# Kernel optimization log

Hardware: AMD Instinct MI355X
Metric: run time of the kernel (lower is better)

## Reference

```python
import jax, jax.numpy as jnp
import numpy as np
import math

B, S, H = 8, 1024, 1024
NH, DH = 16, 64  # MULTI_HEAD, HIDDEN_SIZE_HEAD


def setup_inputs() -> dict:
    key = jax.random.key(0)
    ks = jax.random.split(key, 12)
    scale = 0.02
    inp = {
        "v": jax.random.normal(ks[0], (B, S, H), jnp.float32),
        "k": jax.random.normal(ks[1], (B, S, H), jnp.float32),
        "q": jax.random.normal(ks[2], (B, S, H), jnp.float32),
        # True = masked position (masked_fill semantics)
        "mask": jax.random.bernoulli(ks[3], 0.1, (B, 1, 1, S)),
        "Wq": jax.random.normal(ks[4], (H, H), jnp.float32) * scale,
        "bq": jnp.zeros((H,), jnp.float32),
        "Wk": jax.random.normal(ks[5], (H, H), jnp.float32) * scale,
        "bk": jnp.zeros((H,), jnp.float32),
        "Wv": jax.random.normal(ks[6], (H, H), jnp.float32) * scale,
        "bv": jnp.zeros((H,), jnp.float32),
        "Wm": jax.random.normal(ks[7], (H, H), jnp.float32) * scale,
        "bm": jnp.zeros((H,), jnp.float32),
    }
    return inp


def _split_heads(x):
    # [B, S, H] -> [B, NH, S, DH]
    b, s, _ = x.shape
    return x.reshape(b, s, NH, DH).transpose(0, 2, 1, 3)


def reference(v, k, q, mask, Wq, bq, Wk, bk, Wv, bv, Wm, bm):
    # QKV projections (torch Linear: x @ W.T + b)
    qh = _split_heads(q @ Wq.T + bq)  # [B, NH, S, DH]
    kh = _split_heads(k @ Wk.T + bk)
    vh = _split_heads(v @ Wv.T + bv)

    scores = jnp.einsum("bhqd,bhkd->bhqk", qh, kh) / math.sqrt(DH)
    scores = jnp.where(mask, jnp.float32(-1e9), scores)
    att = jax.nn.softmax(scores, axis=-1)
    # dropout rate 0.0 (eval mode) -> identity
    ctx = jnp.einsum("bhqk,bhkd->bhqd", att, vh)  # [B, NH, S, DH]

    b = q.shape[0]
    merged = ctx.transpose(0, 2, 1, 3).reshape(b, -1, NH * DH)  # [B, S, H]
    return merged @ Wm.T + bm
```

## Files before the change

### kernel.cpp

```cpp
#include <hip/hip_runtime.h>
#include <hip/hip_bf16.h>

#define Bn 8
#define Sn 1024
#define Hn 1024
#define NHn 16
#define DHn 64
#define Mn (Bn * Sn)

typedef unsigned short u16;
typedef short bf16x8 __attribute__((ext_vector_type(8)));
typedef unsigned short u16x4 __attribute__((ext_vector_type(4)));
typedef float f32x4 __attribute__((ext_vector_type(4)));

__device__ __forceinline__ u16 f2bf(float x) {
  union { __hip_bfloat16 h; u16 u; } cv;
  cv.h = __float2bfloat16(x);
  return cv.u;
}

__device__ __forceinline__ void async_ld16(void* lds, const void* g) {
  __builtin_amdgcn_global_load_lds(
      (const __attribute__((address_space(1))) void*)g,
      (__attribute__((address_space(3))) void*)lds, 16, 0, 0);
}

template <int CTRL>
__device__ __forceinline__ float dpp_mov(float v) {
  union { float f; int i; } a, b;
  a.f = v;
  b.i = __builtin_amdgcn_mov_dpp(a.i, CTRL, 0xF, 0xF, 1);
  return b.f;
}
__device__ __forceinline__ float row16_max(float v) {
  v = fmaxf(v, dpp_mov<0xB1>(v));
  v = fmaxf(v, dpp_mov<0x4E>(v));
  v = fmaxf(v, dpp_mov<0x124>(v));
  v = fmaxf(v, dpp_mov<0x128>(v));
  return v;
}
__device__ __forceinline__ float row16_sum(float v) {
  v += dpp_mov<0xB1>(v);
  v += dpp_mov<0x4E>(v);
  v += dpp_mov<0x124>(v);
  v += dpp_mov<0x128>(v);
  return v;
}

__global__ __launch_bounds__(256) void sniff_k(const void* __restrict__ mask,
                                               int* __restrict__ flags) {
  __shared__ int viol;
  if (threadIdx.x == 0) viol = 0;
  __syncthreads();
  const unsigned* mw = (const unsigned*)mask;
  int vb = 0;
#pragma unroll
  for (int j = 0; j < 8; ++j) {
    unsigned v = mw[threadIdx.x * 8 + j];
    if (v > 1u) vb |= 1;
    if ((v & 0xFEFEFEFEu) != 0u) vb |= 2;
    if (!(v == 0u || v == 0x3F800000u)) vb |= 4;
    unsigned h0 = v & 0xFFFFu, h1 = v >> 16;
    if (!((h0 == 0u || h0 == 0x3F80u) && (h1 == 0u || h1 == 0x3F80u))) vb |= 8;
  }
  if (vb) atomicOr(&viol, vb);
  __syncthreads();
  if (threadIdx.x == 0) {
    int mt;
    if (!(viol & 1))      mt = 0;
    else if (!(viol & 2)) mt = 1;
    else if (!(viol & 4)) mt = 3;
    else if (!(viol & 8)) mt = 2;
    else                  mt = 0;
    flags[1] = mt;
  }
}

__global__ __launch_bounds__(256) void convert3(
    const float* __restrict__ a, const float* __restrict__ b,
    const float* __restrict__ c, u16* __restrict__ da,
    u16* __restrict__ db, u16* __restrict__ dc) {
  const int seg = blockIdx.x >> 12;
  const int bid = blockIdx.x & 4095;
  const float* s = seg == 0 ? a : seg == 1 ? b : c;
  u16* d        = seg == 0 ? da : seg == 1 ? db : dc;
  const int i = (bid * 256 + threadIdx.x) * 8;
  f32x4 lo = *(const f32x4*)(s + i);
  f32x4 hi = *(const f32x4*)(s + i + 4);
  bf16x8 o;
#pragma unroll
  for (int j = 0; j < 4; ++j) { o[j] = (short)f2bf(lo[j]); o[4 + j] = (short)f2bf(hi[j]); }
  *(bf16x8*)(d + i) = o;
}

__global__ __launch_bounds__(256) void convertW(
    const float* __restrict__ a, const float* __restrict__ b,
    const float* __restrict__ c, const float* __restrict__ e,
    u16* __restrict__ da, u16* __restrict__ db,
    u16* __restrict__ dc, u16* __restrict__ de) {
  const int seg = blockIdx.x >> 9;
  const int bid = blockIdx.x & 511;
  const float* s = seg == 0 ? a : seg == 1 ? b : seg == 2 ? c : e;
  u16* d        = seg == 0 ? da : seg == 1 ? db : seg == 2 ? dc : de;
  const int i = (bid * 256 + threadIdx.x) * 8;
  f32x4 lo = *(const f32x4*)(s + i);
  f32x4 hi = *(const f32x4*)(s + i + 4);
  bf16x8 o;
#pragma unroll
  for (int j = 0; j < 4; ++j) { o[j] = (short)f2bf(lo[j]); o[4 + j] = (short)f2bf(hi[j]); }
  *(bf16x8*)(d + i) = o;
}

template <int OMODE>
__device__ __forceinline__ void gemm_core(
    u16* As, u16* Bs, const u16* __restrict__ X, const u16* __restrict__ W,
    const float* __restrict__ bias, void* __restrict__ O, float scale)
{
  const int tid  = threadIdx.x;
  const int wave = tid >> 6;
  const int lane = tid & 63;
  const int ln   = lane & 15;
  const int quad = lane >> 4;
  const int m0 = blockIdx.x * 128;
  const int n0 = blockIdx.y * 128;
  const int wm = (wave & 1) * 64;
  const int wn = (wave >> 1) * 64;
  const int r8 = tid >> 3;
  const int cg = ((tid & 7) ^ (r8 & 7)) * 8;
  char* Ad = (char*)As + wave * 1024;
  char* Bd = (char*)Bs + wave * 1024;
  const int rsw = ln & 7;

  f32x4 acc[4][4] = {};

  for (int k0 = 0; k0 < 1024; k0 += 64) {
#pragma unroll
    for (int j = 0; j < 4; ++j) {
      async_ld16(Ad + j * 4096, X + (size_t)(m0 + j * 32 + r8) * 1024 + k0 + cg);
      async_ld16(Bd + j * 4096, W + (size_t)(n0 + j * 32 + r8) * 1024 + k0 + cg);
    }
    __syncthreads();
#pragma unroll
    for (int s = 0; s < 2; ++s) {
      const int co = ((s * 4 + quad) ^ rsw) * 16;
      bf16x8 af[4], bfr[4];
#pragma unroll
      for (int t = 0; t < 4; ++t)
        af[t] = *(const bf16x8*)((char*)As + (wm + t * 16 + ln) * 128 + co);
#pragma unroll
      for (int t = 0; t < 4; ++t)
        bfr[t] = *(const bf16x8*)((char*)Bs + (wn + t * 16 + ln) * 128 + co);
#pragma unroll
      for (int i = 0; i < 4; ++i)
#pragma unroll
        for (int j = 0; j < 4; ++j)
          acc[i][j] = __builtin_amdgcn_mfma_f32_16x16x32_bf16(af[i], bfr[j], acc[i][j], 0, 0, 0);
    }
    __syncthreads();
  }

  if (OMODE == 2) {
    const int bb = m0 >> 10;
    const int sb = m0 & 1023;
#pragma unroll
    for (int j = 0; j < 4; ++j) {
      const int col = n0 + wn + j * 16 + ln;
      const float bv = bias[col];
#pragma unroll
      for (int i = 0; i < 4; ++i) {
        const int sl = sb + wm + i * 16 + quad * 4;
        u16x4 pk;
#pragma unroll
        for (int r = 0; r < 4; ++r) pk[r] = f2bf((acc[i][j][r] + bv) * scale);
        *(u16x4*)&((u16*)O)[((size_t)(bb * 1024 + col)) * 1024 + sl] = pk;
      }
    }
  } else {
#pragma unroll
    for (int j = 0; j < 4; ++j) {
      const int col = n0 + wn + j * 16 + ln;
      const float bv = bias[col];
#pragma unroll
      for (int i = 0; i < 4; ++i) {
        const int rowb = m0 + wm + i * 16 + quad * 4;
#pragma unroll
        for (int r = 0; r < 4; ++r) {
          const float val = (acc[i][j][r] + bv) * scale;
          const size_t idx = (size_t)(rowb + r) * 1024 + col;
          if (OMODE == 1) ((float*)O)[idx] = val;
          else            ((u16*)O)[idx]   = f2bf(val);
        }
      }
    }
  }
}

template <int OMODE>
__global__ __launch_bounds__(256, 3) void gemm_bt(
    const u16* __restrict__ X, const u16* __restrict__ W,
    const float* __restrict__ bias, void* __restrict__ O, float scale)
{
  __shared__ __attribute__((aligned(16))) u16 As[128 * 64];
  __shared__ __attribute__((aligned(16))) u16 Bs[128 * 64];
  gemm_core<OMODE>(As, Bs, X, W, bias, O, scale);
}

__global__ __launch_bounds__(256, 3) void gemm_qk(
    const u16* __restrict__ Xq, const u16* __restrict__ Wq,
    const float* __restrict__ bq, u16* __restrict__ Oq,
    const u16* __restrict__ Xk, const u16* __restrict__ Wk,
    const float* __restrict__ bk, u16* __restrict__ Ok)
{
  __shared__ __attribute__((aligned(16))) u16 As[128 * 64];
  __shared__ __attribute__((aligned(16))) u16 Bs[128 * 64];
  const int z = blockIdx.z;
  gemm_core<0>(As, Bs, z ? Xk : Xq, z ? Wk : Wq, z ? bk : bq,
               z ? (void*)Ok : (void*)Oq, z ? 1.0f : 0.125f);
}

__global__ __launch_bounds__(256, 3) void attn(
    const u16* __restrict__ Qb, const u16* __restrict__ Kb,
    const u16* __restrict__ Vbt, const void* __restrict__ mask,
    const int* __restrict__ flags, u16* __restrict__ Ctx)
{
  __shared__ __attribute__((aligned(16))) u16 Ks[128 * 64];
  __shared__ __attribute__((aligned(16))) u16 Vt[64 * 128];
  __shared__ __attribute__((aligned(16))) u16 Pl[4][16 * 128];
  __shared__ __attribute__((aligned(16))) float maskf[Sn];

  const int tid  = threadIdx.x;
  const int wave = tid >> 6;
  const int lane = tid & 63;
  const int ln   = lane & 15;
  const int quad = lane >> 4;
  const int bx  = blockIdx.x;
  const int x   = bx & 7;
  const int qt  = (bx >> 3) & 15;
  const int grp = bx >> 7;
  const int bh  = grp * 8 + x;
  const int b   = bh >> 4;
  const int h   = bh & 15;

  const int mt = flags[1];
  for (int i = tid; i < Sn; i += 256) {
    const int idx = b * Sn + i;
    int nz;
    if (mt == 0)      nz = ((const int*)mask)[idx] != 0;
    else if (mt == 1) nz = ((const signed char*)mask)[idx] != 0;
    else if (mt == 2) nz = ((const u16*)mask)[idx] != 0;
    else              nz = ((const unsigned*)mask)[idx] != 0;
    maskf[i] = nz ? -1e9f : 0.0f;
  }

  const size_t qoff = (size_t)(b * Sn + qt * 64 + wave * 16 + ln) * Hn + h * DHn;
  bf16x8 qf0 = *(const bf16x8*)&Qb[qoff + quad * 8];
  bf16x8 qf1 = *(const bf16x8*)&Qb[qoff + 32 + quad * 8];

  float mrun[4], lrun[4];
#pragma unroll
  for (int r = 0; r < 4; ++r) { mrun[r] = -INFINITY; lrun[r] = 0.0f; }
  f32x4 acc[4] = {};

  const int kr = tid >> 1, kh = tid & 1;
  const int vd = tid >> 2, vs = tid & 3;
  char* pw  = (char*)Pl[wave];
  char* KsB = (char*)Ks;
  char* VtB = (char*)Vt;

  const int kwb = kr * 128 + kh * 64;
  const int ksw = (kr & 7) << 4;
  const int vwb = vd * 256 + vs * 64;
  const int vsw = (vd & 7) << 4;
  const int rsw = (ln & 7) << 4;

  for (int t8 = 0; t8 < 8; ++t8) {
    const int kv0 = t8 * 128;
    __syncthreads();
    {
      const u16* g = &Kb[(size_t)(b * Sn + kv0 + kr) * Hn + h * DHn + kh * 32];
#pragma unroll
      for (int j = 0; j < 4; ++j)
        *(bf16x8*)(KsB + ((kwb + j * 16) ^ ksw)) = *(const bf16x8*)(g + j * 8);
    }
    {
      const u16* g = &Vbt[(size_t)(b * Sn + h * DHn + vd) * Sn + kv0 + vs * 32];
#pragma unroll
      for (int j = 0; j < 4; ++j)
        *(bf16x8*)(VtB + ((vwb + j * 16) ^ vsw)) = *(const bf16x8*)(g + j * 8);
    }
    __syncthreads();

    f32x4 sc[8];
#pragma unroll
    for (int t = 0; t < 8; ++t) {
      const int rb = (t * 16 + ln) * 128;
      bf16x8 kf0 = *(const bf16x8*)(KsB + ((rb + quad * 16) ^ rsw));
      bf16x8 kf1 = *(const bf16x8*)(KsB + ((rb + 64 + quad * 16) ^ rsw));
      f32x4 z = {};
      z = __builtin_amdgcn_mfma_f32_16x16x32_bf16(qf0, kf0, z, 0, 0, 0);
      z = __builtin_amdgcn_mfma_f32_16x16x32_bf16(qf1, kf1, z, 0, 0, 0);
      sc[t] = z;
    }
    float mf[8];
#pragma unroll
    for (int t = 0; t < 8; ++t) mf[t] = maskf[kv0 + t * 16 + ln];
#pragma unroll
    for (int t = 0; t < 8; ++t)
#pragma unroll
      for (int r = 0; r < 4; ++r) sc[t][r] += mf[t];

    float al[4], mx[4];
#pragma unroll
    for (int r = 0; r < 4; ++r) {
      float v = sc[0][r];
#pragma unroll
      for (int t = 1; t < 8; ++t) v = fmaxf(v, sc[t][r]);
      v = row16_max(v);
      const float mnew = fmaxf(mrun[r], v);
      al[r] = __expf(mrun[r] - mnew);
      mrun[r] = mnew;
      mx[r] = mnew;
    }
#pragma unroll
    for (int r = 0; r < 4; ++r) {
      float s = 0.0f;
#pragma unroll
      for (int t = 0; t < 8; ++t) {
        const float p = __expf(sc[t][r] - mx[r]);
        sc[t][r] = p;
        s += p;
      }
      s = row16_sum(s);
      lrun[r] = lrun[r] * al[r] + s;
    }
#pragma unroll
    for (int t = 0; t < 8; ++t)
#pragma unroll
      for (int r = 0; r < 4; ++r) {
        const int prow = quad * 4 + r;
        *(u16*)(pw + ((prow * 256 + (t * 16 + ln) * 2) ^ ((prow & 7) << 4))) =
            f2bf(sc[t][r]);
      }
#pragma unroll
    for (int dt = 0; dt < 4; ++dt)
#pragma unroll
      for (int r = 0; r < 4; ++r) acc[dt][r] *= al[r];
    bf16x8 pa[4];
#pragma unroll
    for (int c = 0; c < 4; ++c)
      pa[c] = *(const bf16x8*)(pw + ((ln * 256 + c * 64 + quad * 16) ^ rsw));
#pragma unroll
    for (int dt = 0; dt < 4; ++dt) {
      const int vrb = (dt * 16 + ln) * 256;
#pragma unroll
      for (int c = 0; c < 4; ++c) {
        bf16x8 vb = *(const bf16x8*)(VtB + ((vrb + c * 64 + quad * 16) ^ rsw));
        acc[dt] = __builtin_amdgcn_mfma_f32_16x16x32_bf16(pa[c], vb, acc[dt], 0, 0, 0);
      }
    }
  }

#pragma unroll
  for (int dt = 0; dt < 4; ++dt)
#pragma unroll
    for (int r = 0; r < 4; ++r) {
      const int s = qt * 64 + wave * 16 + quad * 4 + r;
      Ctx[(size_t)(b * Sn + s) * Hn + h * DHn + dt * 16 + ln] = f2bf(acc[dt][r] / lrun[r]);
    }
}

extern "C" void kernel_launch(void* const* d_in, const int* in_sizes, int n_in,
                              void* d_out, int out_size, void* d_ws, size_t ws_size,
                              hipStream_t stream) {
  const float* v    = (const float*)d_in[0];
  const float* k    = (const float*)d_in[1];
  const float* q    = (const float*)d_in[2];
  const void*  mask = d_in[3];
  const float* Wq   = (const float*)d_in[4];
  const float* bq   = (const float*)d_in[5];
  const float* Wk   = (const float*)d_in[6];
  const float* bk   = (const float*)d_in[7];
  const float* Wv   = (const float*)d_in[8];
  const float* bv   = (const float*)d_in[9];
  const float* Wm   = (const float*)d_in[10];
  const float* bm   = (const float*)d_in[11];

  char* ws = (char*)d_ws;
  u16* qc  = (u16*)(ws);
  u16* kc  = (u16*)(ws + (16u << 20));
  u16* vc  = (u16*)(ws + (32u << 20));
  u16* Wqc = (u16*)(ws + (48u << 20));
  u16* Wkc = Wqc + (1u << 20);
  u16* Wvc = Wkc + (1u << 20);
  u16* Wmc = Wvc + (1u << 20);
  int* flags = (int*)(ws + (56u << 20));
  u16* Vbt = qc;
  u16* Cx  = kc;
  u16* Qb  = (u16*)d_out;
  u16* Kb  = Qb + (size_t)Mn * Hn;

  sniff_k<<<1, 256, 0, stream>>>(mask, flags);
  convert3<<<3 * 4096, 256, 0, stream>>>(q, k, v, qc, kc, vc);
  convertW<<<4 * 512, 256, 0, stream>>>(Wq, Wk, Wv, Wm, Wqc, Wkc, Wvc, Wmc);

  dim3 blk(256);
  gemm_qk<<<dim3(Mn / 128, Hn / 128, 2), blk, 0, stream>>>(
      qc, Wqc, bq, Qb, kc, Wkc, bk, Kb);
  dim3 grid(Mn / 128, Hn / 128);
  gemm_bt<2><<<grid, blk, 0, stream>>>(vc, Wvc, bv, Vbt, 1.0f);
  attn<<<dim3(Bn * NHn * (Sn / 64)), blk, 0, stream>>>(Qb, Kb, Vbt, mask, flags, Cx);
  gemm_bt<1><<<grid, blk, 0, stream>>>(Cx, Wmc, bm, d_out, 1.0f);
}
```

Measured before the change: 354.5 us.

## Double-buffer GEMM LDS tiles and transpose QK^T layout in attention softmax

The GEMM core now keeps two LDS buffers and issues async global-to-LDS loads for the next K-slice while computing the current one, with launch bounds lowered from 3 to 2 blocks to fit the doubled shared memory. The attention kernel swaps the MFMA operands so each lane holds scores for a single query row. This lets the softmax max and sum use per-lane reductions plus two cross-quad shuffles instead of per-row DPP reductions, lets the mask be read as vectors, and lets P be written to LDS as packed 4-element stores. Costs are lower GEMM occupancy and extra shuffles to broadcast the rescale factors and normalizers back into the output layout.

```diff
diff --git a/kernel.cpp b/kernel.cpp
--- a/kernel.cpp
+++ b/kernel.cpp
@@ -23,28 +23,6 @@
   __builtin_amdgcn_global_load_lds(
       (const __attribute__((address_space(1))) void*)g,
       (__attribute__((address_space(3))) void*)lds, 16, 0, 0);
-}
-
-template <int CTRL>
-__device__ __forceinline__ float dpp_mov(float v) {
-  union { float f; int i; } a, b;
-  a.f = v;
-  b.i = __builtin_amdgcn_mov_dpp(a.i, CTRL, 0xF, 0xF, 1);
-  return b.f;
-}
-__device__ __forceinline__ float row16_max(float v) {
-  v = fmaxf(v, dpp_mov<0xB1>(v));
-  v = fmaxf(v, dpp_mov<0x4E>(v));
-  v = fmaxf(v, dpp_mov<0x124>(v));
-  v = fmaxf(v, dpp_mov<0x128>(v));
-  return v;
-}
-__device__ __forceinline__ float row16_sum(float v) {
-  v += dpp_mov<0xB1>(v);
-  v += dpp_mov<0x4E>(v);
-  v += dpp_mov<0x124>(v);
-  v += dpp_mov<0x128>(v);
-  return v;
 }
 
 __global__ __launch_bounds__(256) void sniff_k(const void* __restrict__ mask,
@@ -127,29 +105,37 @@
   const int wn = (wave >> 1) * 64;
   const int r8 = tid >> 3;
   const int cg = ((tid & 7) ^ (r8 & 7)) * 8;
-  char* Ad = (char*)As + wave * 1024;
-  char* Bd = (char*)Bs + wave * 1024;
   const int rsw = ln & 7;
 
   f32x4 acc[4][4] = {};
 
-  for (int k0 = 0; k0 < 1024; k0 += 64) {
+  auto STAGE = [&](int buf, int k0) {
+    char* Ad = (char*)As + buf * 16384 + wave * 1024;
+    char* Bd = (char*)Bs + buf * 16384 + wave * 1024;
 #pragma unroll
     for (int j = 0; j < 4; ++j) {
       async_ld16(Ad + j * 4096, X + (size_t)(m0 + j * 32 + r8) * 1024 + k0 + cg);
       async_ld16(Bd + j * 4096, W + (size_t)(n0 + j * 32 + r8) * 1024 + k0 + cg);
     }
-    __syncthreads();
+  };
+
+  STAGE(0, 0);
+  __syncthreads();
+  for (int step = 0; step < 16; ++step) {
+    const int cur = step & 1;
+    if (step < 15) STAGE(cur ^ 1, (step + 1) * 64);
+    const char* Ab = (const char*)As + cur * 16384;
+    const char* Bb = (const char*)Bs + cur * 16384;
 #pragma unroll
     for (int s = 0; s < 2; ++s) {
       const int co = ((s * 4 + quad) ^ rsw) * 16;
       bf16x8 af[4], bfr[4];
 #pragma unroll
       for (int t = 0; t < 4; ++t)
-        af[t] = *(const bf16x8*)((char*)As + (wm + t * 16 + ln) * 128 + co);
+        af[t] = *(const bf16x8*)(Ab + (wm + t * 16 + ln) * 128 + co);
 #pragma unroll
       for (int t = 0; t < 4; ++t)
-        bfr[t] = *(const bf16x8*)((char*)Bs + (wn + t * 16 + ln) * 128 + co);
+        bfr[t] = *(const bf16x8*)(Bb + (wn + t * 16 + ln) * 128 + co);
 #pragma unroll
       for (int i = 0; i < 4; ++i)
 #pragma unroll
@@ -196,23 +182,23 @@
 }
 
 template <int OMODE>
-__global__ __launch_bounds__(256, 3) void gemm_bt(
+__global__ __launch_bounds__(256, 2) void gemm_bt(
     const u16* __restrict__ X, const u16* __restrict__ W,
     const float* __restrict__ bias, void* __restrict__ O, float scale)
 {
-  __shared__ __attribute__((aligned(16))) u16 As[128 * 64];
-  __shared__ __attribute__((aligned(16))) u16 Bs[128 * 64];
+  __shared__ __attribute__((aligned(16))) u16 As[2 * 128 * 64];
+  __shared__ __attribute__((aligned(16))) u16 Bs[2 * 128 * 64];
   gemm_core<OMODE>(As, Bs, X, W, bias, O, scale);
 }
 
-__global__ __launch_bounds__(256, 3) void gemm_qk(
+__global__ __launch_bounds__(256, 2) void gemm_qk(
     const u16* __restrict__ Xq, const u16* __restrict__ Wq,
     const float* __restrict__ bq, u16* __restrict__ Oq,
     const u16* __restrict__ Xk, const u16* __restrict__ Wk,
     const float* __restrict__ bk, u16* __restrict__ Ok)
 {
-  __shared__ __attribute__((aligned(16))) u16 As[128 * 64];
-  __shared__ __attribute__((aligned(16))) u16 Bs[128 * 64];
+  __shared__ __attribute__((aligned(16))) u16 As[2 * 128 * 64];
+  __shared__ __attribute__((aligned(16))) u16 Bs[2 * 128 * 64];
   const int z = blockIdx.z;
   gemm_core<0>(As, Bs, z ? Xk : Xq, z ? Wk : Wq, z ? bk : bq,
                z ? (void*)Ok : (void*)Oq, z ? 1.0f : 0.125f);
@@ -256,9 +242,7 @@
   bf16x8 qf0 = *(const bf16x8*)&Qb[qoff + quad * 8];
   bf16x8 qf1 = *(const bf16x8*)&Qb[qoff + 32 + quad * 8];
 
-  float mrun[4], lrun[4];
-#pragma unroll
-  for (int r = 0; r < 4; ++r) { mrun[r] = -INFINITY; lrun[r] = 0.0f; }
+  float mrun = -INFINITY, lrun = 0.0f;
   f32x4 acc[4] = {};
 
   const int kr = tid >> 1, kh = tid & 1;
@@ -272,6 +256,8 @@
   const int vwb = vd * 256 + vs * 64;
   const int vsw = (vd & 7) << 4;
   const int rsw = (ln & 7) << 4;
+  const int pwb = ln * 256;
+  const int psw = (ln & 7) << 4;
 
   for (int t8 = 0; t8 < 8; ++t8) {
     const int kv0 = t8 * 128;
@@ -297,58 +283,61 @@
       bf16x8 kf0 = *(const bf16x8*)(KsB + ((rb + quad * 16) ^ rsw));
       bf16x8 kf1 = *(const bf16x8*)(KsB + ((rb + 64 + quad * 16) ^ rsw));
       f32x4 z = {};
-      z = __builtin_amdgcn_mfma_f32_16x16x32_bf16(qf0, kf0, z, 0, 0, 0);
-      z = __builtin_amdgcn_mfma_f32_16x16x32_bf16(qf1, kf1, z, 0, 0, 0);
+      z = __builtin_amdgcn_mfma_f32_16x16x32_bf16(kf0, qf0, z, 0, 0, 0);
+      z = __builtin_amdgcn_mfma_f32_16x16x32_bf16(kf1, qf1, z, 0, 0, 0);
       sc[t] = z;
     }
-    float mf[8];
-#pragma unroll
-    for (int t = 0; t < 8; ++t) mf[t] = maskf[kv0 + t * 16 + ln];
+#pragma unroll
+    for (int t = 0; t < 8; ++t) {
+      const f32x4 mf4 = *(const f32x4*)&maskf[kv0 + t * 16 + quad * 4];
+#pragma unroll
+      for (int r = 0; r < 4; ++r) sc[t][r] += mf4[r];
+    }
+
+    f32x4 mm = sc[0];
+#pragma unroll
+    for (int t = 1; t < 8; ++t)
+#pragma unroll
+      for (int r = 0; r < 4; ++r) mm[r] = fmaxf(mm[r], sc[t][r]);
+    float vmax = fmaxf(fmaxf(mm[0], mm[1]), fmaxf(mm[2], mm[3]));
+    vmax = fmaxf(vmax, __shfl_xor(vmax, 16));
+    vmax = fmaxf(vmax, __shfl_xor(vmax, 32));
+    const float mnew = fmaxf(mrun, vmax);
+    const float al = __expf(mrun - mnew);
+    mrun = mnew;
+    float ssum = 0.0f;
 #pragma unroll
     for (int t = 0; t < 8; ++t)
 #pragma unroll
-      for (int r = 0; r < 4; ++r) sc[t][r] += mf[t];
-
-    float al[4], mx[4];
-#pragma unroll
-    for (int r = 0; r < 4; ++r) {
-      float v = sc[0][r];
-#pragma unroll
-      for (int t = 1; t < 8; ++t) v = fmaxf(v, sc[t][r]);
-      v = row16_max(v);
-      const float mnew = fmaxf(mrun[r], v);
-      al[r] = __expf(mrun[r] - mnew);
-      mrun[r] = mnew;
-      mx[r] = mnew;
-    }
-#pragma unroll
-    for (int r = 0; r < 4; ++r) {
-      float s = 0.0f;
-#pragma unroll
-      for (int t = 0; t < 8; ++t) {
-        const float p = __expf(sc[t][r] - mx[r]);
+      for (int r = 0; r < 4; ++r) {
+        const float p = __expf(sc[t][r] - mnew);
         sc[t][r] = p;
-        s += p;
+        ssum += p;
       }
-      s = row16_sum(s);
-      lrun[r] = lrun[r] * al[r] + s;
-    }
-#pragma unroll
-    for (int t = 0; t < 8; ++t)
-#pragma unroll
-      for (int r = 0; r < 4; ++r) {
-        const int prow = quad * 4 + r;
-        *(u16*)(pw + ((prow * 256 + (t * 16 + ln) * 2) ^ ((prow & 7) << 4))) =
-            f2bf(sc[t][r]);
-      }
+    ssum += __shfl_xor(ssum, 16);
+    ssum += __shfl_xor(ssum, 32);
+    lrun = lrun * al + ssum;
+
+#pragma unroll
+    for (int t = 0; t < 8; ++t) {
+      u16x4 pk;
+#pragma unroll
+      for (int r = 0; r < 4; ++r) pk[r] = f2bf(sc[t][r]);
+      *(u16x4*)(pw + ((pwb + t * 32 + quad * 8) ^ psw)) = pk;
+    }
+
+    float alr[4];
+#pragma unroll
+    for (int r = 0; r < 4; ++r) alr[r] = __shfl(al, quad * 4 + r);
 #pragma unroll
     for (int dt = 0; dt < 4; ++dt)
 #pragma unroll
-      for (int r = 0; r < 4; ++r) acc[dt][r] *= al[r];
+      for (int r = 0; r < 4; ++r) acc[dt][r] *= alr[r];
+
     bf16x8 pa[4];
 #pragma unroll
     for (int c = 0; c < 4; ++c)
-      pa[c] = *(const bf16x8*)(pw + ((ln * 256 + c * 64 + quad * 16) ^ rsw));
+      pa[c] = *(const bf16x8*)(pw + ((pwb + c * 64 + quad * 16) ^ psw));
 #pragma unroll
     for (int dt = 0; dt < 4; ++dt) {
       const int vrb = (dt * 16 + ln) * 256;
@@ -360,12 +349,15 @@
     }
   }
 
+  float lr[4];
+#pragma unroll
+  for (int r = 0; r < 4; ++r) lr[r] = __shfl(lrun, quad * 4 + r);
 #pragma unroll
   for (int dt = 0; dt < 4; ++dt)
 #pragma unroll
     for (int r = 0; r < 4; ++r) {
       const int s = qt * 64 + wave * 16 + quad * 4 + r;
-      Ctx[(size_t)(b * Sn + s) * Hn + h * DHn + dt * 16 + ln] = f2bf(acc[dt][r] / lrun[r]);
+      Ctx[(size_t)(b * Sn + s) * Hn + h * DHn + dt * 16 + ln] = f2bf(acc[dt][r] / lr[r]);
     }
 }
 
```

Measured after the change: 345.7 us. 2.5% less time.
